# Kernel optimization log

Hardware: AMD Instinct MI355X
Metric: run time of the kernel (lower is better)

The kernel has to match this reference:

```python
import jax, jax.numpy as jnp
import numpy as np

N_E = 1024
E_DIM = 256
BETA = 0.25


def setup_inputs() -> dict:
    key = jax.random.key(0)
    k1, k2 = jax.random.split(key)
    z = jax.random.normal(k1, (16, 256, 64, 64), dtype=jnp.float32)
    # embedding initialized uniform(-1/n_e, 1/n_e)
    emb = jax.random.uniform(k2, (N_E, E_DIM), dtype=jnp.float32,
                             minval=-1.0 / N_E, maxval=1.0 / N_E)
    return {"z": z, "emb": emb}


def reference(z, emb):
    # z: [B, C, H, W] with C == e_dim; emb: [n_e, e_dim]
    z_perm = jnp.transpose(z, (0, 2, 3, 1))            # [B, H, W, C]
    zf = z_perm.reshape(-1, E_DIM)                      # [N, C]

    # pairwise squared distances: ||z||^2 + ||e||^2 - 2 z e^T  -> [N, n_e]
    d = (jnp.sum(zf * zf, axis=1, keepdims=True)
         + jnp.sum(emb * emb, axis=1)
         - 2.0 * jnp.matmul(zf, emb.T))

    idx = jnp.argmin(d, axis=1)                         # [N]
    zq_flat = emb[idx]                                  # gather [N, C]
    z_q = zq_flat.reshape(z_perm.shape)                 # [B, H, W, C]

    one_hot = jax.nn.one_hot(idx, N_E, dtype=jnp.float32)  # [N, n_e]

    codebook_loss = jnp.mean((jax.lax.stop_gradient(z_q) - z_perm) ** 2)
    commitment_loss = jnp.mean((z_q - jax.lax.stop_gradient(z_perm)) ** 2)
    loss = codebook_loss + BETA * commitment_loss

    # straight-through estimator
    z_q = z_perm + jax.lax.stop_gradient(z_q - z_perm)

    e_mean = jnp.mean(one_hot, axis=0)                  # [n_e]
    perplexity = jnp.exp(-jnp.sum(e_mean * jnp.log(e_mean + 1e-10)))

    z_q = jnp.transpose(z_q, (0, 3, 1, 2))              # [B, C, H, W]
    idx_ret = idx[:, None]
    return (z_q, loss, perplexity, one_hot, idx_ret, d)
```

## Files before the change

kernel.cpp:

```cpp
#include <hip/hip_runtime.h>
#include <math.h>


typedef unsigned short ushort;
typedef unsigned int uint;
typedef __attribute__((ext_vector_type(8))) short  bf16x8;
typedef __attribute__((ext_vector_type(8))) ushort ushort8v;
typedef __attribute__((ext_vector_type(4))) float  f32x4;

static const size_t O_LOSS = 16777216;
static const size_t O_PERP = 16777217;
static const size_t O_OH   = 16777218;
static const size_t O_IDX  = 83886082;
static const size_t O_D    = 83951618;

static const size_t WS_ENORM = 0;
static const size_t WS_ZNF   = 4096;
static const size_t WS_IDX   = 266240;
static const size_t WS_HIST  = 528384;
static const size_t WS_FCNT  = 532480;
static const size_t WS_FROWS = 532496;
static const size_t WS_LOSS  = 794640;
static const size_t WS_BHI   = 798736;

#define THR_FLAG 4e-4f

__device__ __forceinline__ ushort f2bf(float f) {
  uint u = __float_as_uint(f);
  return (ushort)((u + 0x7FFFu + ((u >> 16) & 1u)) >> 16);
}
__device__ __forceinline__ void gload16(const void* g, void* l) {
  __builtin_amdgcn_global_load_lds(
      (const __attribute__((address_space(1))) void*)g,
      (__attribute__((address_space(3))) void*)l, 16, 0, 0);
}

__global__ __launch_bounds__(256) void vq_prep_e(const float* __restrict__ emb,
    float* __restrict__ enormf, ushort* __restrict__ Bhi,
    int* __restrict__ hist, int* __restrict__ flag_cnt) {
  const int j = blockIdx.x * 256 + threadIdx.x;
  hist[j] = 0;
  if (j == 0) *flag_cnt = 0;
  const float* e = emb + ((size_t)j << 8);
  ushort* br = Bhi + ((size_t)j << 8);
  double s = 0.0;
  for (int k0 = 0; k0 < 256; k0 += 8) {
    const float4 a = *(const float4*)&e[k0];
    const float4 b = *(const float4*)&e[k0 + 4];
    ushort8v v;
    v[0] = f2bf(a.x); v[1] = f2bf(a.y); v[2] = f2bf(a.z); v[3] = f2bf(a.w);
    v[4] = f2bf(b.x); v[5] = f2bf(b.y); v[6] = f2bf(b.z); v[7] = f2bf(b.w);
    *(ushort8v*)&br[k0] = v;
    s += (double)a.x * (double)a.x;  s += (double)a.y * (double)a.y;
    s += (double)a.z * (double)a.z;  s += (double)a.w * (double)a.w;
    s += (double)b.x * (double)b.x;  s += (double)b.y * (double)b.y;
    s += (double)b.z * (double)b.z;  s += (double)b.w * (double)b.w;
  }
  enormf[j] = (float)s;
}

__global__ __launch_bounds__(512, 4) void vq_mega(const float* __restrict__ z,
    const float* __restrict__ emb, const ushort* __restrict__ Bhi,
    const float* __restrict__ enormf, float* __restrict__ out,
    int* __restrict__ idxw, float* __restrict__ znf,
    int* __restrict__ hist, int* __restrict__ flag_cnt, int* __restrict__ flag_rows,
    double* __restrict__ loss_part) {
  __shared__ ushort As[32768];
  __shared__ ushort Bs[2][4096];

  const int t = threadIdx.x;
  const int lane = t & 63;
  const int w = t >> 6;
  const int wr = w >> 1, wc = w & 1;
  const int g = lane >> 4, cl = lane & 15;
  const int blk = blockIdx.x;
  const int m0 = blk << 7;
  const int zb = blk >> 5;
  const int r0 = (blk & 31) << 7;
  float* dmat = out + O_D;

  float* Fs = (float*)&Bs[0][0];
  const int kk = t >> 5, rq = t & 31;
  const int arow = t >> 2, gq = t & 3;
  const int swzr = (arow & 7) << 3;
  double zn2 = 0.0;
  for (int kc = 0; kc < 256; kc += 32) {
    const float4 v0 = *(const float4*)&z[((size_t)zb << 20) + ((size_t)(kc + kk) << 12) + r0 + (rq << 2)];
    const float4 v1 = *(const float4*)&z[((size_t)zb << 20) + ((size_t)(kc + kk + 16) << 12) + r0 + (rq << 2)];
    if (kc) __syncthreads();
    *(float4*)&Fs[(kk << 7) + (rq << 2)] = v0;
    *(float4*)&Fs[((kk + 16) << 7) + (rq << 2)] = v1;
    __syncthreads();
    ushort8v pk;
#pragma unroll
    for (int j = 0; j < 8; ++j) {
      const float v = Fs[(((gq << 3) + j) << 7) | arow];
      zn2 += (double)v * (double)v;
      pk[j] = f2bf(v);
    }
    *(ushort8v*)&As[(arow << 8) + ((kc + (gq << 3)) ^ swzr)] = pk;
  }
  __syncthreads();
  {
    double* znp = (double*)&Bs[0][0];
    znp[(arow << 2) + gq] = zn2;
  }
  __syncthreads();
  float* znf_s = (float*)((char*)&Bs[0][0] + 8192);
  if (t < 128) {
    const double* zp = (const double*)&Bs[0][0] + (t << 2);
    const float zf = (float)(zp[0] + zp[1] + zp[2] + zp[3]);
    znf[m0 + t] = zf;
    znf_s[t] = zf;
  }
  __syncthreads();
  float zn_[2][4];
#pragma unroll
  for (int ai = 0; ai < 2; ++ai)
#pragma unroll
    for (int rg = 0; rg < 4; ++rg)
      zn_[ai][rg] = znf_s[(wr << 5) + (ai << 4) + (g << 2) + rg];
  gload16(Bhi + ((size_t)(t >> 2) << 8) + ((t & 3) << 3), &Bs[0][t << 3]);

  f32x4 acc[2][4];
#pragma unroll
  for (int a = 0; a < 2; ++a)
#pragma unroll
    for (int b = 0; b < 4; ++b) acc[a][b] = (f32x4)(0.0f);
  float run1[8], run2[8]; int runi[8];
#pragma unroll
  for (int r = 0; r < 8; ++r) { run1[r] = 3.0e38f; run2[r] = 3.0e38f; runi[r] = 0; }

  __syncthreads();

  int cur = 0;
  for (int it = 0; it < 64; ++it) {
    const int nt = it >> 3, kch = it & 7;
    if (it < 63) {
      const int nit = it + 1;
      gload16(Bhi + ((size_t)(nit >> 3) << 15) + ((nit & 7) << 5) +
                  ((size_t)(t >> 2) << 8) + ((t & 3) << 3),
              &Bs[cur ^ 1][t << 3]);
    }
    {
      const int kb = kch << 5;
      bf16x8 av[2], bv[4];
#pragma unroll
      for (int ai = 0; ai < 2; ++ai) {
        const int row = (wr << 5) + (ai << 4) + cl;
        av[ai] = *(const bf16x8*)&As[(row << 8) + ((kb + (g << 3)) ^ ((cl & 7) << 3))];
      }
#pragma unroll
      for (int bj = 0; bj < 4; ++bj)
        bv[bj] = *(const bf16x8*)&Bs[cur][(((wc << 6) + (bj << 4) + cl) << 5) + (g << 3)];
#pragma unroll
      for (int ai = 0; ai < 2; ++ai)
#pragma unroll
        for (int bj = 0; bj < 4; ++bj)
          acc[ai][bj] = __builtin_amdgcn_mfma_f32_16x16x32_bf16(av[ai], bv[bj], acc[ai][bj], 0, 0, 0);
    }
    if (kch == 7) {
      float en_[4];
#pragma unroll
      for (int bj = 0; bj < 4; ++bj)
        en_[bj] = enormf[(nt << 7) + (wc << 6) + (bj << 4) + cl];
#pragma unroll
      for (int ai = 0; ai < 2; ++ai) {
#pragma unroll
        for (int bj = 0; bj < 4; ++bj) {
          const int n = (nt << 7) + (wc << 6) + (bj << 4) + cl;
#pragma unroll
          for (int rg = 0; rg < 4; ++rg) {
            const float S = zn_[ai][rg] + en_[bj];
            const float v = S - 2.0f * acc[ai][bj][rg];
            const int m = m0 + (wr << 5) + (ai << 4) + (g << 2) + rg;
            dmat[((size_t)m << 10) + n] = v;
            const int rr = (ai << 2) + rg;
            if (v < run1[rr]) { run2[rr] = run1[rr]; run1[rr] = v; runi[rr] = n; }
            else if (v < run2[rr]) { run2[rr] = v; }
          }
          acc[ai][bj] = (f32x4)(0.0f);
        }
      }
    }
    __syncthreads();
    cur ^= 1;
  }

  float*  sd1  = (float*)&Bs[0][0];
  int*    si1  = (int*)((char*)&Bs[0][0] + 1024);
  float*  sd2  = (float*)((char*)&Bs[0][0] + 2048);
  int*    idxs = (int*)((char*)&Bs[0][0] + 3072);
  double* red  = (double*)((char*)&Bs[0][0] + 3584);

#pragma unroll
  for (int rr = 0; rr < 8; ++rr) {
    float a1 = run1[rr], a2 = run2[rr]; int ai1 = runi[rr];
    for (int off = 8; off >= 1; off >>= 1) {
      const float o1 = __shfl_xor(a1, off, 16);
      const int   oi = __shfl_xor(ai1, off, 16);
      const float o2 = __shfl_xor(a2, off, 16);
      const float ns = fminf(fminf(a2, o2), fmaxf(a1, o1));
      if (o1 < a1 || (o1 == a1 && oi < ai1)) { a1 = o1; ai1 = oi; }
      a2 = ns;
    }
    if (cl == 0) {
      const int r = (wr << 5) + ((rr >> 2) << 4) + (g << 2) + (rr & 3);
      sd1[(r << 1) + wc] = a1; si1[(r << 1) + wc] = ai1; sd2[(r << 1) + wc] = a2;
    }
  }
  __syncthreads();
  if (t < 128) {
    const float a1 = sd1[t << 1], b1 = sd1[(t << 1) + 1];
    const int ai1 = si1[t << 1], bi1 = si1[(t << 1) + 1];
    const float a2 = sd2[t << 1], b2 = sd2[(t << 1) + 1];
    float d1, d2; int i1;
    if (b1 < a1 || (b1 == a1 && bi1 < ai1)) { d1 = b1; i1 = bi1; d2 = fminf(a1, b2); }
    else { d1 = a1; i1 = ai1; d2 = fminf(b1, a2); }
    const int m = m0 + t;
    idxw[m] = i1; idxs[t] = i1;
    out[O_IDX + m] = (float)i1;
    atomicAdd(&hist[i1], 1);
    if (d2 - d1 < THR_FLAG) {
      const int p = atomicAdd(flag_cnt, 1);
      flag_rows[p] = m;
    }
    red[t] = (double)d1;
  }
  __syncthreads();
  for (int off = 64; off > 0; off >>= 1) {
    if (t < off) red[t] += red[t + off];
    __syncthreads();
  }
  if (t == 0) loss_part[blk] = red[0];

  float2* ohbase = (float2*)(out + O_OH);
  for (int rr = 0; rr < 16; ++rr) {
    const int r = (w << 4) + rr;
    const int idx = idxs[r];
    float2* row = ohbase + (((size_t)(m0 + r)) << 9);
    const int half = idx >> 1;
#pragma unroll
    for (int i = 0; i < 8; ++i) {
      const int slot = (i << 6) + lane;
      float2 v; v.x = 0.0f; v.y = 0.0f;
      if (slot == half) { if (idx & 1) v.y = 1.0f; else v.x = 1.0f; }
      row[slot] = v;
    }
  }

  float* Et = (float*)As;
  for (int ch = 0; ch < 4; ++ch) {
    __syncthreads();
    {
      const int e = idxs[arow];
#pragma unroll
      for (int j2 = 0; j2 < 4; ++j2) {
        const int cb = (gq << 4) + (j2 << 2);
        const float4 ev = *(const float4*)&emb[((size_t)e << 8) + (ch << 6) + cb];
        Et[(cb + 0) * 132 + arow] = ev.x;
        Et[(cb + 1) * 132 + arow] = ev.y;
        Et[(cb + 2) * 132 + arow] = ev.z;
        Et[(cb + 3) * 132 + arow] = ev.w;
      }
    }
    __syncthreads();
#pragma unroll
    for (int i = 0; i < 8; ++i) {
      const int cll = (w << 3) + i;
      const int c = (ch << 6) + cll;
#pragma unroll
      for (int h = 0; h < 2; ++h) {
        const int rr = (h << 6) + lane;
        out[((size_t)zb << 20) + ((size_t)c << 12) + r0 + rr] = Et[cll * 132 + rr];
      }
    }
  }
}

__global__ __launch_bounds__(256) void vq_refine(const float* __restrict__ z,
    const float* __restrict__ emb, const float* __restrict__ znf,
    const float* __restrict__ enormf, const int* __restrict__ flag_cnt,
    const int* __restrict__ flag_rows, int* __restrict__ idxw,
    float* __restrict__ out, int* __restrict__ hist) {
  __shared__ float zrow[256];
  __shared__ float dmin_s[4];
  __shared__ int cand[256];
  __shared__ int ncand_s;
  __shared__ int old_s;
  __shared__ float rv[256];
  __shared__ int ri[256];
  const float* dmat = out + O_D;
  const int t = threadIdx.x;
  const int n = *flag_cnt;
  for (int f = blockIdx.x; f < n; f += gridDim.x) {
    const int m = flag_rows[f];
    __syncthreads();
    if (t == 0) { ncand_s = 0; old_s = idxw[m]; }
    zrow[t] = z[(((size_t)(m >> 12)) << 20) + (size_t)(m & 4095) + ((size_t)t << 12)];
    const float* dr = dmat + ((size_t)m << 10);
    const float2 a = *(const float2*)&dr[t << 2];
    const float2 b = *(const float2*)&dr[(t << 2) + 2];
    float dmin = fminf(fminf(a.x, a.y), fminf(b.x, b.y));
    for (int off = 32; off >= 1; off >>= 1) dmin = fminf(dmin, __shfl_xor(dmin, off));
    if ((t & 63) == 0) dmin_s[t >> 6] = dmin;
    __syncthreads();
    dmin = fminf(fminf(dmin_s[0], dmin_s[1]), fminf(dmin_s[2], dmin_s[3]));
    const float lim = dmin + THR_FLAG;
    const float dv[4] = {a.x, a.y, b.x, b.y};
#pragma unroll
    for (int q = 0; q < 4; ++q)
      if (dv[q] <= lim) {
        const int p = atomicAdd(&ncand_s, 1);
        if (p < 256) cand[p] = (t << 2) + q;
      }
    __syncthreads();
    const int nc = min(ncand_s, 256);
    float best = 3.0e38f; int bi = 1 << 30;
    if (t < nc) {
      const int j = cand[t];
      const float* er = emb + ((size_t)j << 8);
      float s = 0.0f;
      for (int k = 0; k < 256; ++k) s = fmaf(zrow[k], er[k], s);
      const float S = znf[m] + enormf[j];
      best = S - 2.0f * s;
      bi = j;
    }
    rv[t] = best; ri[t] = bi;
    __syncthreads();
    for (int off = 128; off > 0; off >>= 1) {
      if (t < off) {
        const float ov = rv[t + off]; const int oi = ri[t + off];
        if (ov < rv[t] || (ov == rv[t] && oi < ri[t])) { rv[t] = ov; ri[t] = oi; }
      }
      __syncthreads();
    }
    const int nbi = ri[0];
    const int old = old_s;
    if (nbi != old) {
      if (t == 0) {
        idxw[m] = nbi;
        out[O_IDX + m] = (float)nbi;
        out[O_OH + ((size_t)m << 10) + (size_t)old] = 0.0f;
        out[O_OH + ((size_t)m << 10) + (size_t)nbi] = 1.0f;
        atomicAdd(&hist[old], -1);
        atomicAdd(&hist[nbi], 1);
      }
      out[(((size_t)(m >> 12)) << 20) + ((size_t)t << 12) + (size_t)(m & 4095)] =
          emb[((size_t)nbi << 8) + t];
    }
  }
}

__global__ __launch_bounds__(256) void vq_final(const double* __restrict__ loss_part,
    const int* __restrict__ hist, float* __restrict__ out) {
  __shared__ double red[256];
  const int t = threadIdx.x;
  red[t] = loss_part[t] + loss_part[t + 256];
  __syncthreads();
  for (int off = 128; off > 0; off >>= 1) {
    if (t < off) red[t] += red[t + off];
    __syncthreads();
  }
  if (t == 0) out[O_LOSS] = (float)(1.25 * red[0] / 16777216.0);
  __syncthreads();
  double h = 0.0;
  for (int i = t; i < 1024; i += 256) {
    const double p = (double)hist[i] / 65536.0;
    h += p * log(p + 1e-10);
  }
  red[t] = h;
  __syncthreads();
  for (int off = 128; off > 0; off >>= 1) {
    if (t < off) red[t] += red[t + off];
    __syncthreads();
  }
  if (t == 0) out[O_PERP] = (float)exp(-red[0]);
}

extern "C" void kernel_launch(void* const* d_in, const int* in_sizes, int n_in,
                              void* d_out, int out_size, void* d_ws, size_t ws_size,
                              hipStream_t stream) {
  const float* z   = (const float*)d_in[0];
  const float* emb = (const float*)d_in[1];
  float* out = (float*)d_out;
  char* ws = (char*)d_ws;

  float*  enormf    = (float*)(ws + WS_ENORM);
  float*  znf       = (float*)(ws + WS_ZNF);
  int*    idxw      = (int*)(ws + WS_IDX);
  int*    hist      = (int*)(ws + WS_HIST);
  int*    flag_cnt  = (int*)(ws + WS_FCNT);
  int*    flag_rows = (int*)(ws + WS_FROWS);
  double* loss_part = (double*)(ws + WS_LOSS);
  ushort* Bhi       = (ushort*)(ws + WS_BHI);

  vq_prep_e<<<4, 256, 0, stream>>>(emb, enormf, Bhi, hist, flag_cnt);
  vq_mega<<<512, 512, 0, stream>>>(z, emb, Bhi, enormf, out, idxw, znf, hist,
                                   flag_cnt, flag_rows, loss_part);
  vq_refine<<<4096, 256, 0, stream>>>(z, emb, znf, enormf, flag_cnt, flag_rows,
                                      idxw, out, hist);
  vq_final<<<1, 256, 0, stream>>>(loss_part, hist, out);
}
```

Measured before the change: 334.2 us.

## Stream codebook B fragments from global, prefetch z chunks, and swap MFMA operands

The main GEMM loop no longer stages codebook tiles in LDS with double-buffered global_load_lds and per-iteration barriers. Each wave now reads its bf16 codebook fragments straight from global/L2 and runs the inner k loop without synchronisation. The MFMA operands are swapped so each lane holds four consecutive codebook columns, which allows float2 stores of the distance matrix and a float4 load of the embedding norms. The z transpose prologue gains a two-chunk-ahead register prefetch, and __syncthreads is replaced by a custom barrier that waits only on LDS counters. The cost is more global/L2 traffic for B, which every block re-reads, and a barrier that relies on no outstanding vector-memory dependencies.

```diff
diff --git a/kernel.cpp b/kernel.cpp
--- a/kernel.cpp
+++ b/kernel.cpp
@@ -29,10 +29,13 @@
   uint u = __float_as_uint(f);
   return (ushort)((u + 0x7FFFu + ((u >> 16) & 1u)) >> 16);
 }
-__device__ __forceinline__ void gload16(const void* g, void* l) {
-  __builtin_amdgcn_global_load_lds(
-      (const __attribute__((address_space(1))) void*)g,
-      (__attribute__((address_space(3))) void*)l, 16, 0, 0);
+
+__device__ __forceinline__ void bar() {
+  __builtin_amdgcn_sched_barrier(0);
+  asm volatile("s_waitcnt lgkmcnt(0)" ::: "memory");
+  __builtin_amdgcn_sched_barrier(0);
+  __builtin_amdgcn_s_barrier();
+  __builtin_amdgcn_sched_barrier(0);
 }
 
 __global__ __launch_bounds__(256) void vq_prep_e(const float* __restrict__ emb,
@@ -66,7 +69,7 @@
     int* __restrict__ hist, int* __restrict__ flag_cnt, int* __restrict__ flag_rows,
     double* __restrict__ loss_part) {
   __shared__ ushort As[32768];
-  __shared__ ushort Bs[2][4096];
+  __shared__ float  Fs[4096];
 
   const int t = threadIdx.x;
   const int lane = t & 63;
@@ -79,18 +82,27 @@
   const int r0 = (blk & 31) << 7;
   float* dmat = out + O_D;
 
-  float* Fs = (float*)&Bs[0][0];
   const int kk = t >> 5, rq = t & 31;
   const int arow = t >> 2, gq = t & 3;
   const int swzr = (arow & 7) << 3;
+  const float* zbase = z + ((size_t)zb << 20) + r0 + (rq << 2);
+  float4 va0 = *(const float4*)(zbase + ((size_t)(kk) << 12));
+  float4 va1 = *(const float4*)(zbase + ((size_t)(kk + 16) << 12));
+  float4 vb0 = *(const float4*)(zbase + ((size_t)(32 + kk) << 12));
+  float4 vb1 = *(const float4*)(zbase + ((size_t)(32 + kk + 16) << 12));
   double zn2 = 0.0;
-  for (int kc = 0; kc < 256; kc += 32) {
-    const float4 v0 = *(const float4*)&z[((size_t)zb << 20) + ((size_t)(kc + kk) << 12) + r0 + (rq << 2)];
-    const float4 v1 = *(const float4*)&z[((size_t)zb << 20) + ((size_t)(kc + kk + 16) << 12) + r0 + (rq << 2)];
-    if (kc) __syncthreads();
-    *(float4*)&Fs[(kk << 7) + (rq << 2)] = v0;
-    *(float4*)&Fs[((kk + 16) << 7) + (rq << 2)] = v1;
-    __syncthreads();
+#pragma unroll
+  for (int c = 0; c < 8; ++c) {
+    float4 vc0, vc1;
+    if (c < 6) {
+      vc0 = *(const float4*)(zbase + ((size_t)(((c + 2) << 5) + kk) << 12));
+      vc1 = *(const float4*)(zbase + ((size_t)(((c + 2) << 5) + kk + 16) << 12));
+    }
+    if (c) bar();
+    *(float4*)&Fs[(kk << 7) + (rq << 2)] = va0;
+    *(float4*)&Fs[((kk + 16) << 7) + (rq << 2)] = va1;
+    bar();
+    const int kc = c << 5;
     ushort8v pk;
 #pragma unroll
     for (int j = 0; j < 8; ++j) {
@@ -99,117 +111,106 @@
       pk[j] = f2bf(v);
     }
     *(ushort8v*)&As[(arow << 8) + ((kc + (gq << 3)) ^ swzr)] = pk;
-  }
-  __syncthreads();
+    va0 = vb0; va1 = vb1; vb0 = vc0; vb1 = vc1;
+  }
+  bar();
   {
-    double* znp = (double*)&Bs[0][0];
+    double* znp = (double*)Fs;
     znp[(arow << 2) + gq] = zn2;
   }
-  __syncthreads();
-  float* znf_s = (float*)((char*)&Bs[0][0] + 8192);
+  bar();
+  float* znf_s = Fs + 2048;
   if (t < 128) {
-    const double* zp = (const double*)&Bs[0][0] + (t << 2);
+    const double* zp = (const double*)Fs + (t << 2);
     const float zf = (float)(zp[0] + zp[1] + zp[2] + zp[3]);
     znf[m0 + t] = zf;
     znf_s[t] = zf;
   }
-  __syncthreads();
-  float zn_[2][4];
-#pragma unroll
-  for (int ai = 0; ai < 2; ++ai)
-#pragma unroll
-    for (int rg = 0; rg < 4; ++rg)
-      zn_[ai][rg] = znf_s[(wr << 5) + (ai << 4) + (g << 2) + rg];
-  gload16(Bhi + ((size_t)(t >> 2) << 8) + ((t & 3) << 3), &Bs[0][t << 3]);
-
-  f32x4 acc[2][4];
-#pragma unroll
-  for (int a = 0; a < 2; ++a)
-#pragma unroll
-    for (int b = 0; b < 4; ++b) acc[a][b] = (f32x4)(0.0f);
-  float run1[8], run2[8]; int runi[8];
-#pragma unroll
-  for (int r = 0; r < 8; ++r) { run1[r] = 3.0e38f; run2[r] = 3.0e38f; runi[r] = 0; }
-
-  __syncthreads();
-
-  int cur = 0;
-  for (int it = 0; it < 64; ++it) {
-    const int nt = it >> 3, kch = it & 7;
-    if (it < 63) {
-      const int nit = it + 1;
-      gload16(Bhi + ((size_t)(nit >> 3) << 15) + ((nit & 7) << 5) +
-                  ((size_t)(t >> 2) << 8) + ((t & 3) << 3),
-              &Bs[cur ^ 1][t << 3]);
-    }
-    {
+  bar();
+
+  const float zn_0 = znf_s[(wr << 5) + cl];
+  const float zn_1 = znf_s[(wr << 5) + 16 + cl];
+  const ushort* bptr[4];
+#pragma unroll
+  for (int bj = 0; bj < 4; ++bj)
+    bptr[bj] = Bhi + ((((wc << 6) + (bj << 4) + cl) << 8) + (g << 3));
+  float* drow0 = dmat + ((size_t)(m0 + (wr << 5) + cl) << 10);
+  float* drow1 = dmat + ((size_t)(m0 + (wr << 5) + 16 + cl) << 10);
+  const int arow0 = ((wr << 5) + cl) << 8;
+  const int arow1 = ((wr << 5) + 16 + cl) << 8;
+  const int avswz = (cl & 7) << 3;
+
+  f32x4 acc[4][2];
+#pragma unroll
+  for (int bj = 0; bj < 4; ++bj) { acc[bj][0] = (f32x4)(0.0f); acc[bj][1] = (f32x4)(0.0f); }
+  float run1[2], run2[2]; int runi[2];
+  run1[0] = run1[1] = 3.0e38f; run2[0] = run2[1] = 3.0e38f; runi[0] = runi[1] = 0;
+
+  for (int nt = 0; nt < 8; ++nt) {
+#pragma unroll
+    for (int kch = 0; kch < 8; ++kch) {
       const int kb = kch << 5;
-      bf16x8 av[2], bv[4];
+      const int ks = (kb + (g << 3)) ^ avswz;
+      bf16x8 av0 = *(const bf16x8*)&As[arow0 + ks];
+      bf16x8 av1 = *(const bf16x8*)&As[arow1 + ks];
+      bf16x8 bv[4];
+#pragma unroll
+      for (int bj = 0; bj < 4; ++bj)
+        bv[bj] = *(const bf16x8*)(bptr[bj] + (nt << 15) + kb);
+#pragma unroll
+      for (int bj = 0; bj < 4; ++bj) {
+        acc[bj][0] = __builtin_amdgcn_mfma_f32_16x16x32_bf16(bv[bj], av0, acc[bj][0], 0, 0, 0);
+        acc[bj][1] = __builtin_amdgcn_mfma_f32_16x16x32_bf16(bv[bj], av1, acc[bj][1], 0, 0, 0);
+      }
+    }
+    const int nb0 = (nt << 7) + (wc << 6) + (g << 2);
+#pragma unroll
+    for (int bj = 0; bj < 4; ++bj) {
+      const float4 en4 = *(const float4*)&enormf[nb0 + (bj << 4)];
+      const float en_r[4] = {en4.x, en4.y, en4.z, en4.w};
 #pragma unroll
       for (int ai = 0; ai < 2; ++ai) {
-        const int row = (wr << 5) + (ai << 4) + cl;
-        av[ai] = *(const bf16x8*)&As[(row << 8) + ((kb + (g << 3)) ^ ((cl & 7) << 3))];
-      }
-#pragma unroll
-      for (int bj = 0; bj < 4; ++bj)
-        bv[bj] = *(const bf16x8*)&Bs[cur][(((wc << 6) + (bj << 4) + cl) << 5) + (g << 3)];
-#pragma unroll
-      for (int ai = 0; ai < 2; ++ai)
-#pragma unroll
-        for (int bj = 0; bj < 4; ++bj)
-          acc[ai][bj] = __builtin_amdgcn_mfma_f32_16x16x32_bf16(av[ai], bv[bj], acc[ai][bj], 0, 0, 0);
-    }
-    if (kch == 7) {
-      float en_[4];
-#pragma unroll
-      for (int bj = 0; bj < 4; ++bj)
-        en_[bj] = enormf[(nt << 7) + (wc << 6) + (bj << 4) + cl];
-#pragma unroll
-      for (int ai = 0; ai < 2; ++ai) {
-#pragma unroll
-        for (int bj = 0; bj < 4; ++bj) {
-          const int n = (nt << 7) + (wc << 6) + (bj << 4) + cl;
-#pragma unroll
-          for (int rg = 0; rg < 4; ++rg) {
-            const float S = zn_[ai][rg] + en_[bj];
-            const float v = S - 2.0f * acc[ai][bj][rg];
-            const int m = m0 + (wr << 5) + (ai << 4) + (g << 2) + rg;
-            dmat[((size_t)m << 10) + n] = v;
-            const int rr = (ai << 2) + rg;
-            if (v < run1[rr]) { run2[rr] = run1[rr]; run1[rr] = v; runi[rr] = n; }
-            else if (v < run2[rr]) { run2[rr] = v; }
-          }
-          acc[ai][bj] = (f32x4)(0.0f);
+        const float znv = ai ? zn_1 : zn_0;
+        float dv[4];
+#pragma unroll
+        for (int rg = 0; rg < 4; ++rg) {
+          dv[rg] = (znv + en_r[rg]) - 2.0f * acc[bj][ai][rg];
+          const int n = nb0 + (bj << 4) + rg;
+          if (dv[rg] < run1[ai]) { run2[ai] = run1[ai]; run1[ai] = dv[rg]; runi[ai] = n; }
+          else if (dv[rg] < run2[ai]) { run2[ai] = dv[rg]; }
         }
-      }
-    }
-    __syncthreads();
-    cur ^= 1;
-  }
-
-  float*  sd1  = (float*)&Bs[0][0];
-  int*    si1  = (int*)((char*)&Bs[0][0] + 1024);
-  float*  sd2  = (float*)((char*)&Bs[0][0] + 2048);
-  int*    idxs = (int*)((char*)&Bs[0][0] + 3072);
-  double* red  = (double*)((char*)&Bs[0][0] + 3584);
-
-#pragma unroll
-  for (int rr = 0; rr < 8; ++rr) {
-    float a1 = run1[rr], a2 = run2[rr]; int ai1 = runi[rr];
-    for (int off = 8; off >= 1; off >>= 1) {
-      const float o1 = __shfl_xor(a1, off, 16);
-      const int   oi = __shfl_xor(ai1, off, 16);
-      const float o2 = __shfl_xor(a2, off, 16);
+        float2* dst = (float2*)((ai ? drow1 : drow0) + nb0 + (bj << 4));
+        dst[0] = make_float2(dv[0], dv[1]);
+        dst[1] = make_float2(dv[2], dv[3]);
+        acc[bj][ai] = (f32x4)(0.0f);
+      }
+    }
+  }
+
+  float*  sd1  = Fs;
+  int*    si1  = (int*)(Fs + 256);
+  float*  sd2  = Fs + 512;
+  int*    idxs = (int*)(Fs + 768);
+  double* red  = (double*)(Fs + 896);
+
+#pragma unroll
+  for (int ai = 0; ai < 2; ++ai) {
+    float a1 = run1[ai], a2 = run2[ai]; int i1 = runi[ai];
+#pragma unroll
+    for (int off = 16; off <= 32; off <<= 1) {
+      const float o1 = __shfl_xor(a1, off);
+      const int   oi = __shfl_xor(i1, off);
+      const float o2 = __shfl_xor(a2, off);
       const float ns = fminf(fminf(a2, o2), fmaxf(a1, o1));
-      if (o1 < a1 || (o1 == a1 && oi < ai1)) { a1 = o1; ai1 = oi; }
+      if (o1 < a1 || (o1 == a1 && oi < i1)) { a1 = o1; i1 = oi; }
       a2 = ns;
     }
-    if (cl == 0) {
-      const int r = (wr << 5) + ((rr >> 2) << 4) + (g << 2) + (rr & 3);
-      sd1[(r << 1) + wc] = a1; si1[(r << 1) + wc] = ai1; sd2[(r << 1) + wc] = a2;
-    }
-  }
-  __syncthreads();
+    if (g == 0) {
+      const int r = (wr << 5) + (ai << 4) + cl;
+      sd1[(r << 1) + wc] = a1; si1[(r << 1) + wc] = i1; sd2[(r << 1) + wc] = a2;
+    }
+  }
+  bar();
   if (t < 128) {
     const float a1 = sd1[t << 1], b1 = sd1[(t << 1) + 1];
     const int ai1 = si1[t << 1], bi1 = si1[(t << 1) + 1];
@@ -227,10 +228,10 @@
     }
     red[t] = (double)d1;
   }
-  __syncthreads();
+  bar();
   for (int off = 64; off > 0; off >>= 1) {
     if (t < off) red[t] += red[t + off];
-    __syncthreads();
+    bar();
   }
   if (t == 0) loss_part[blk] = red[0];
 
@@ -251,7 +252,7 @@
 
   float* Et = (float*)As;
   for (int ch = 0; ch < 4; ++ch) {
-    __syncthreads();
+    bar();
     {
       const int e = idxs[arow];
 #pragma unroll
@@ -264,7 +265,7 @@
         Et[(cb + 3) * 132 + arow] = ev.w;
       }
     }
-    __syncthreads();
+    bar();
 #pragma unroll
     for (int i = 0; i < 8; ++i) {
       const int cll = (w << 3) + i;
```

New measurement: 380.0 us. +13.7%, slower.
